# Kernel tuning notes

Measured on AMD Instinct MI355X. Metric: run time of the kernel, lower is better.

## Reference

```python
import jax, jax.numpy as jnp
import numpy as np

MAX_POS = 1024  # config.max_position_embeddings
NUM_HEADS = 16
HEAD_DIM = 64


def setup_inputs() -> dict:
    key = jax.random.key(0)
    ks = jax.random.split(key, 4)
    B, S, H = 4, 1024, 1024
    return {
        "hidden_states": jax.random.normal(ks[0], (B, S, H), dtype=jnp.float32),
        "qkv_w": jax.random.normal(ks[1], (3 * H, H), dtype=jnp.float32) * 0.02,
        "qkv_b": jax.random.normal(ks[2], (3 * H,), dtype=jnp.float32) * 0.02,
        "dist_emb": jax.random.normal(ks[3], (2 * MAX_POS - 1, HEAD_DIM), dtype=jnp.float32) * 0.02,
        "ext_mask": jnp.zeros((B, 1, 1, S), dtype=jnp.float32),
    }


def reference(hidden_states, qkv_w, qkv_b, dist_emb, ext_mask):
    B, S, H = hidden_states.shape
    h, d = NUM_HEADS, HEAD_DIM
    # fused QKV projection (q|k|v concatenated on output dim)
    qkv = jnp.einsum('bsi,oi->bso', hidden_states, qkv_w) + qkv_b
    q, k, v = jnp.split(qkv, 3, axis=-1)
    to_heads = lambda x: x.reshape(B, S, h, d).transpose(0, 2, 1, 3)  # [B,h,S,d]
    q, k, v = to_heads(q), to_heads(k), to_heads(v)
    # raw attention scores [B,h,S,S]
    scores = jnp.einsum('bhld,bhrd->bhlr', q, k)
    # relative_key_query positional bias
    pos = jnp.arange(S)
    distance = pos[:, None] - pos[None, :]          # [S,S]
    pe = dist_emb[distance + MAX_POS - 1]           # [S,S,d]
    scores = scores + jnp.einsum('bhld,lrd->bhlr', q, pe) \
                    + jnp.einsum('bhrd,lrd->bhlr', k, pe)
    scores = scores / jnp.sqrt(jnp.asarray(d, scores.dtype))
    scores = scores + ext_mask
    probs = jax.nn.softmax(scores, axis=-1)
    ctx = jnp.einsum('bhlr,bhrd->bhld', probs, v)   # [B,h,S,d]
    return ctx.transpose(0, 2, 1, 3).reshape(B, S, h * d)
```

## Files before the change

### kernel.cpp

```cpp
#include <hip/hip_runtime.h>
#include <hip/hip_bf16.h>

#define SEQ 1024
#define NH  16

typedef __attribute__((ext_vector_type(8))) short short8;
typedef __attribute__((ext_vector_type(4))) float floatx4;
typedef __attribute__((ext_vector_type(4))) unsigned short ushortx4;

#define GLDS16(gp, lp) __builtin_amdgcn_global_load_lds( \
    (const __attribute__((address_space(1))) void*)(gp), \
    (__attribute__((address_space(3))) void*)(lp), 16, 0, 0)

__device__ __forceinline__ unsigned short f2b(float f) {
    union { __hip_bfloat16 h; unsigned short u; } v;
    v.h = __float2bfloat16(f);
    return v.u;
}
__device__ __forceinline__ float b2f(unsigned short h) {
    union { unsigned u; float f; } v; v.u = ((unsigned)h) << 16;
    return v.f;
}

#define TADDR(base, row, ch) ((base) + ((row) << 6) + ((((ch) ^ ((row) & 7))) << 3))

__global__ void cast_kernel(const float* __restrict__ hs, const float* __restrict__ W,
                            const float* __restrict__ E,
                            unsigned short* __restrict__ hsb,
                            unsigned short* __restrict__ Wb,
                            unsigned short* __restrict__ Eb)
{
    const int QH = 1048576, QW = 786432, QE = 32752;
    const int NT = QH + QW + QE;
    for (int q = blockIdx.x * 256 + threadIdx.x; q < NT; q += gridDim.x * 256) {
        const float* src; unsigned short* dst; int off;
        if (q < QH)           { src = hs; dst = hsb; off = q; }
        else if (q < QH + QW) { src = W;  dst = Wb;  off = q - QH; }
        else                  { src = E;  dst = Eb;  off = q - QH - QW; }
        const float4 v = *(const float4*)(src + (size_t)off * 4);
        ushortx4 o; o[0] = f2b(v.x); o[1] = f2b(v.y); o[2] = f2b(v.z); o[3] = f2b(v.w);
        *(ushortx4*)(dst + (size_t)off * 4) = o;
    }
}

__global__ __launch_bounds__(256, 3) void qkv_gemm(
    const unsigned short* __restrict__ Ab, const unsigned short* __restrict__ Bb,
    const float* __restrict__ bias,
    unsigned short* __restrict__ Qb, unsigned short* __restrict__ Kb,
    unsigned short* __restrict__ Vt)
{
    __shared__ unsigned short sm[16384];
    const int t = threadIdx.x, w = t >> 6;
    const int ln = t & 15, g = (t >> 4) & 3;
    const int wm = w >> 1, wn = w & 1;
    const int bid = blockIdx.x + blockIdx.y * 24;
    const int swzid = (bid & 7) * 96 + (bid >> 3);
    const int m0 = (swzid / 24) << 7, o0 = (swzid % 24) << 7;

    floatx4 acc[4][4];
#pragma unroll
    for (int i = 0; i < 4; ++i)
#pragma unroll
        for (int j = 0; j < 4; ++j) acc[i][j] = (floatx4){0.f, 0.f, 0.f, 0.f};

    auto stage = [&](int kb, int buf) {
        const int base = buf << 14;
#pragma unroll
        for (int p = 0; p < 2; ++p) {
            const int idx = (p << 8) + t;
            const int row = idx >> 2;
            const int c = (idx & 3) ^ ((row ^ (row >> 2)) & 3);
            GLDS16(Ab + (size_t)(m0 + row) * 1024 + kb + (c << 3),
                   (char*)sm + base + (p << 12) + (w << 10));
            GLDS16(Bb + (size_t)(o0 + row) * 1024 + kb + (c << 3),
                   (char*)sm + base + 8192 + (p << 12) + (w << 10));
        }
    };

    stage(0, 0);
    __syncthreads();
    int buf = 0;
    for (int kb = 0; kb < 1024; kb += 32) {
        if (kb + 32 < 1024) stage(kb + 32, buf ^ 1);
        const int be = buf << 13;
        short8 af[4], bf_[4];
#pragma unroll
        for (int i = 0; i < 4; ++i) {
            const int r = (wm << 6) + (i << 4) + ln;
            af[i] = *(const short8*)&sm[be + (r << 5) + ((g ^ ((r ^ (r >> 2)) & 3)) << 3)];
        }
#pragma unroll
        for (int j = 0; j < 4; ++j) {
            const int r = (wn << 6) + (j << 4) + ln;
            bf_[j] = *(const short8*)&sm[be + 4096 + (r << 5) + ((g ^ ((r ^ (r >> 2)) & 3)) << 3)];
        }
#pragma unroll
        for (int i = 0; i < 4; ++i)
#pragma unroll
            for (int j = 0; j < 4; ++j)
                acc[i][j] = __builtin_amdgcn_mfma_f32_16x16x32_bf16(af[i], bf_[j], acc[i][j], 0, 0, 0);
        __syncthreads();
        buf ^= 1;
    }

    const int which = o0 >> 10;
    float bj[4];
#pragma unroll
    for (int j = 0; j < 4; ++j) bj[j] = bias[o0 + (wn << 6) + (j << 4) + ln];
    const int b0 = m0 >> 10;

    if (which == 2) {
#pragma unroll
        for (int i = 0; i < 4; ++i)
#pragma unroll
            for (int j = 0; j < 4; ++j) {
                const int oi = (wn << 6) + (j << 4) + ln;
                const int sb = oi & 15;
#pragma unroll
                for (int q = 0; q < 4; ++q) {
                    const int mi = (wm << 6) + (i << 4) + (g << 2) + q;
                    sm[(oi << 7) + ((((mi >> 3) ^ sb)) << 3) + (mi & 7)] =
                        f2b(acc[i][j][q] + bj[j]);
                }
            }
        __syncthreads();
#pragma unroll
        for (int it = 0; it < 8; ++it) {
            const int c = (it << 8) + t;
            const int oi = c >> 4, mi0 = (c & 15) << 3;
            const short8 v = *(const short8*)&sm[(oi << 7) + ((((mi0 >> 3) ^ (oi & 15))) << 3)];
            const int hh = ((o0 >> 6) + (oi >> 6)) & 15;
            const int d = oi & 63;
            const int s0 = (m0 & 1023) + mi0;
            *(short8*)(Vt + (((size_t)((b0 << 4) + hh)) << 16) + (d << 10) + s0) = v;
        }
    } else {
        unsigned short* dst = which ? Kb : Qb;
        const float sc = which ? 1.0f : 0.125f;
#pragma unroll
        for (int i = 0; i < 4; ++i)
#pragma unroll
            for (int j = 0; j < 4; ++j) {
                const int oi = (wn << 6) + (j << 4) + ln;
#pragma unroll
                for (int q = 0; q < 4; ++q) {
                    const int mi = (wm << 6) + (i << 4) + (g << 2) + q;
                    sm[(mi << 7) + oi] = f2b((acc[i][j][q] + bj[j]) * sc);
                }
            }
        __syncthreads();
#pragma unroll
        for (int it = 0; it < 8; ++it) {
            const int c = (it << 8) + t;
            const int mi = c >> 4, oi0 = (c & 15) << 3;
            const short8 v = *(const short8*)&sm[(mi << 7) + oi0];
            const int s = (m0 & 1023) + mi;
            const int hh = ((o0 >> 6) + (oi0 >> 6)) & 15;
            const int d0 = oi0 & 63;
            *(short8*)(dst + (((size_t)((b0 << 4) + hh)) << 16) + (s << 6) + d0) = v;
        }
    }
}

__global__ __launch_bounds__(256, 3) void attn_mfma(
    const unsigned short* __restrict__ Qb, const unsigned short* __restrict__ Kb,
    const unsigned short* __restrict__ Vt, const unsigned short* __restrict__ Eb,
    const float* __restrict__ mask, float* __restrict__ outp)
{
    __shared__ __align__(16) unsigned short sm[25600];
    const int t = threadIdx.x, w = t >> 6;
    const int wu = __builtin_amdgcn_readfirstlane(w);
    const int ln = t & 15, g = (t >> 4) & 3;
    const int bid = blockIdx.x;
    const int swz = ((bid & 7) << 7) | (bid >> 3);
    const int bh = swz >> 4;
    const int l0 = (swz & 15) << 6;
    const int b = bh >> 4, h = bh & 15;
    const size_t hb = (size_t)bh << 16;
    const int x0 = (w << 4) + (g << 2);

    const int qr = (w << 4) + ln;
    const short8 qa0 = *(const short8*)(Qb + hb + ((size_t)(l0 + qr) << 6) + (g << 3));
    const short8 qa1 = *(const short8*)(Qb + hb + ((size_t)(l0 + qr) << 6) + 32 + (g << 3));

    floatx4 O[4];
    float mr[4], lr[4];
#pragma unroll
    for (int dt = 0; dt < 4; ++dt) O[dt] = (floatx4){0.f, 0.f, 0.f, 0.f};
#pragma unroll
    for (int q = 0; q < 4; ++q) { mr[q] = -1e30f; lr[q] = 0.f; }

    for (int r0 = 0; r0 < SEQ; r0 += 64) {
        __syncthreads();
#pragma unroll
        for (int p = 0; p < 2; ++p) {
            const int idx = (p << 8) + t;
            const int row = idx >> 3;
            const int c = (idx & 7) ^ (row & 7);
            GLDS16(Kb + hb + ((size_t)(r0 + row) << 6) + (c << 3),
                   (char*)sm + (p << 12) + (w << 10));
        }
        const int j0 = l0 - r0 + 960;
#pragma unroll
        for (int p = 0; p < 4; ++p) {
            const int idx = (p << 8) + t;
            const int row = idx >> 3;
            const int c = (idx & 7) ^ (row & 7);
            GLDS16(Eb + ((size_t)(j0 + row) << 6) + (c << 3),
                   (char*)sm + 8192 + (p << 12) + (w << 10));
        }
        __syncthreads();
        short8 kf[4][2];
#pragma unroll
        for (int j = 0; j < 4; ++j) {
            const int kr = (j << 4) + ln;
            kf[j][0] = *(const short8*)&sm[TADDR(0, kr, g)];
            kf[j][1] = *(const short8*)&sm[TADDR(0, kr, 4 + g)];
        }
        const int wr = (w << 4) + ln;
        const short8 ka0 = *(const short8*)&sm[TADDR(0, wr, g)];
        const short8 ka1 = *(const short8*)&sm[TADDR(0, wr, 4 + g)];

        floatx4 S[4];
#pragma unroll
        for (int j = 0; j < 4; ++j) {
            floatx4 z = (floatx4){0.f, 0.f, 0.f, 0.f};
            z = __builtin_amdgcn_mfma_f32_16x16x32_bf16(qa0, kf[j][0], z, 0, 0, 0);
            S[j] = __builtin_amdgcn_mfma_f32_16x16x32_bf16(qa1, kf[j][1], z, 0, 0, 0);
        }
#pragma unroll
        for (int dt = 0; dt < 8; ++dt) {
            const bool doU = (dt >= wu) && (dt <= wu + 4);
            const bool doW = (dt >= 3 - wu) && (dt <= 7 - wu);
            if (!doU && !doW) continue;
            const int er = (dt << 4) + ln;
            const short8 e0 = *(const short8*)&sm[TADDR(4096, er, g)];
            const short8 e1 = *(const short8*)&sm[TADDR(4096, er, 4 + g)];
            if (doU) {
                floatx4 z = (floatx4){0.f, 0.f, 0.f, 0.f};
                z = __builtin_amdgcn_mfma_f32_16x16x32_bf16(qa0, e0, z, 0, 0, 0);
                const floatx4 U = __builtin_amdgcn_mfma_f32_16x16x32_bf16(qa1, e1, z, 0, 0, 0);
                int a = 12288 + (x0 - (dt << 4) - ln + 79) * 72 + x0;
#pragma unroll
                for (int q = 0; q < 4; ++q) { sm[a] = f2b(U[q]); a += 73; }
            }
            if (doW) {
                floatx4 z2 = (floatx4){0.f, 0.f, 0.f, 0.f};
                z2 = __builtin_amdgcn_mfma_f32_16x16x32_bf16(ka0, e0, z2, 0, 0, 0);
                const floatx4 Wv = __builtin_amdgcn_mfma_f32_16x16x32_bf16(ka1, e1, z2, 0, 0, 0);
                int a = 19200 + x0 * 101 + (dt << 4) + ln - 47;
#pragma unroll
                for (int q = 0; q < 4; ++q) { sm[a] = f2b(Wv[q] * 0.125f); a += 101; }
            }
        }
        __syncthreads();
#pragma unroll
        for (int p = 0; p < 2; ++p) {
            const int idx = (p << 8) + t;
            const int row = idx >> 3;
            const int c = (idx & 7) ^ (row & 7);
            GLDS16(Vt + hb + ((size_t)row << 10) + r0 + (c << 3),
                   (char*)sm + 8192 + (p << 12) + (w << 10));
        }
        float Pw[4][4];
#pragma unroll
        for (int j = 0; j < 4; ++j) {
            const int rr = (j << 4) + ln;
            const float mk = mask[(b << 10) + r0 + rr];
            const ushortx4 u4 = *(const ushortx4*)&sm[12288 + (rr + 16) * 72 + x0];
            const ushortx4 w4 = *(const ushortx4*)&sm[19200 + rr * 100 + 16 + x0];
#pragma unroll
            for (int q = 0; q < 4; ++q)
                S[j][q] += b2f(u4[q]) + b2f(w4[q]) + mk;
        }
#pragma unroll
        for (int q = 0; q < 4; ++q) {
            float tm = fmaxf(fmaxf(S[0][q], S[1][q]), fmaxf(S[2][q], S[3][q]));
            tm = fmaxf(tm, __shfl_xor(tm, 1));
            tm = fmaxf(tm, __shfl_xor(tm, 2));
            tm = fmaxf(tm, __shfl_xor(tm, 4));
            tm = fmaxf(tm, __shfl_xor(tm, 8));
            const float mnew = fmaxf(mr[q], tm);
            const float al = __expf(mr[q] - mnew);
            float sum = 0.f;
#pragma unroll
            for (int j = 0; j < 4; ++j) {
                const float p = __expf(S[j][q] - mnew);
                Pw[j][q] = p; sum += p;
            }
            sum += __shfl_xor(sum, 1);
            sum += __shfl_xor(sum, 2);
            sum += __shfl_xor(sum, 4);
            sum += __shfl_xor(sum, 8);
            lr[q] = lr[q] * al + sum;
            mr[q] = mnew;
#pragma unroll
            for (int dt = 0; dt < 4; ++dt) O[dt][q] *= al;
        }
#pragma unroll
        for (int j = 0; j < 4; ++j) {
            const int rr = (j << 4) + ln;
#pragma unroll
            for (int q = 0; q < 4; ++q) {
                const int l = x0 + q;
                sm[8192 + (l << 6) + ((((rr >> 3) ^ (l & 7)) << 3)) + (rr & 7)] = f2b(Pw[j][q]);
            }
        }
        __syncthreads();
        const int pr = (w << 4) + ln;
        const short8 pa0 = *(const short8*)&sm[TADDR(8192, pr, g)];
        const short8 pa1 = *(const short8*)&sm[TADDR(8192, pr, 4 + g)];
#pragma unroll
        for (int dt = 0; dt < 4; ++dt) {
            const int vr = (dt << 4) + ln;
            const short8 v0 = *(const short8*)&sm[TADDR(4096, vr, g)];
            const short8 v1 = *(const short8*)&sm[TADDR(4096, vr, 4 + g)];
            O[dt] = __builtin_amdgcn_mfma_f32_16x16x32_bf16(pa0, v0, O[dt], 0, 0, 0);
            O[dt] = __builtin_amdgcn_mfma_f32_16x16x32_bf16(pa1, v1, O[dt], 0, 0, 0);
        }
    }
#pragma unroll
    for (int dt = 0; dt < 4; ++dt)
#pragma unroll
        for (int q = 0; q < 4; ++q) {
            const int l = x0 + q;
            outp[((size_t)b << 20) + ((size_t)(l0 + l) << 10) + (h << 6) + (dt << 4) + ln]
                = O[dt][q] / lr[q];
        }
}

extern "C" void kernel_launch(void* const* d_in, const int* in_sizes, int n_in,
                              void* d_out, int out_size, void* d_ws, size_t ws_size,
                              hipStream_t stream)
{
    const float* hs   = (const float*)d_in[0];
    const float* qkvw = (const float*)d_in[1];
    const float* qkvb = (const float*)d_in[2];
    const float* demb = (const float*)d_in[3];
    const float* mask = (const float*)d_in[4];
    float* out = (float*)d_out;

    char* ws = (char*)d_ws;
    unsigned short* hsb = (unsigned short*)(ws);
    unsigned short* Wb  = (unsigned short*)(ws + 8388608);
    unsigned short* Eb  = (unsigned short*)(ws + 14680064);
    unsigned short* Qb  = (unsigned short*)(ws + 14942208);
    unsigned short* Kb  = (unsigned short*)(ws + 23330816);
    unsigned short* Vt  = (unsigned short*)(ws + 31719424);

    cast_kernel<<<2048, 256, 0, stream>>>(hs, qkvw, demb, hsb, Wb, Eb);
    qkv_gemm<<<dim3(24, 32), 256, 0, stream>>>(hsb, Wb, qkvb, Qb, Kb, Vt);
    attn_mfma<<<1024, 256, 0, stream>>>(Qb, Kb, Vt, Eb, mask, out);
}
```

Baseline: 226.8 us.

## Double-buffer K tiles and compact swizzled layout for relative-position bias staging

K tiles are now double-buffered in shared memory, and the next tile is prefetched during the softmax and PV phase so its load overlaps compute. The U/W positional-bias scratch buffers are repacked into compact 64x64 XOR-swizzled layouts that drop out-of-range entries. This frees LDS for the second K buffer and is meant to reduce bank conflicts on the bias writes and reads. It adds bounds checks on the bias stores and a more involved shared-memory address map.

Result: slower. 324.2 us (+43.0%).

```diff
diff --git a/kernel.cpp b/kernel.cpp
--- a/kernel.cpp
+++ b/kernel.cpp
@@ -167,7 +167,7 @@
     const unsigned short* __restrict__ Vt, const unsigned short* __restrict__ Eb,
     const float* __restrict__ mask, float* __restrict__ outp)
 {
-    __shared__ __align__(16) unsigned short sm[25600];
+    __shared__ __align__(16) unsigned short sm[24576];
     const int t = threadIdx.x, w = t >> 6;
     const int wu = __builtin_amdgcn_readfirstlane(w);
     const int ln = t & 15, g = (t >> 4) & 3;
@@ -178,28 +178,35 @@
     const int b = bh >> 4, h = bh & 15;
     const size_t hb = (size_t)bh << 16;
     const int x0 = (w << 4) + (g << 2);
+    const int cb = x0 >> 2;
 
     const int qr = (w << 4) + ln;
     const short8 qa0 = *(const short8*)(Qb + hb + ((size_t)(l0 + qr) << 6) + (g << 3));
     const short8 qa1 = *(const short8*)(Qb + hb + ((size_t)(l0 + qr) << 6) + 32 + (g << 3));
 
-    floatx4 O[4];
-    float mr[4], lr[4];
-#pragma unroll
-    for (int dt = 0; dt < 4; ++dt) O[dt] = (floatx4){0.f, 0.f, 0.f, 0.f};
-#pragma unroll
-    for (int q = 0; q < 4; ++q) { mr[q] = -1e30f; lr[q] = 0.f; }
-
-    for (int r0 = 0; r0 < SEQ; r0 += 64) {
-        __syncthreads();
+    auto stageK = [&](int rb, int kbuf) {
 #pragma unroll
         for (int p = 0; p < 2; ++p) {
             const int idx = (p << 8) + t;
             const int row = idx >> 3;
             const int c = (idx & 7) ^ (row & 7);
-            GLDS16(Kb + hb + ((size_t)(r0 + row) << 6) + (c << 3),
-                   (char*)sm + (p << 12) + (w << 10));
-        }
+            GLDS16(Kb + hb + ((size_t)(rb + row) << 6) + (c << 3),
+                   (char*)sm + (kbuf << 13) + (p << 12) + (w << 10));
+        }
+    };
+
+    stageK(0, 0);
+
+    floatx4 O[4];
+    float mr[4], lr[4];
+#pragma unroll
+    for (int dt = 0; dt < 4; ++dt) O[dt] = (floatx4){0.f, 0.f, 0.f, 0.f};
+#pragma unroll
+    for (int q = 0; q < 4; ++q) { mr[q] = -1e30f; lr[q] = 0.f; }
+
+    for (int r0 = 0; r0 < SEQ; r0 += 64) {
+        const int kb = (r0 >> 6) & 1;
+        __syncthreads();
         const int j0 = l0 - r0 + 960;
 #pragma unroll
         for (int p = 0; p < 4; ++p) {
@@ -207,19 +214,20 @@
             const int row = idx >> 3;
             const int c = (idx & 7) ^ (row & 7);
             GLDS16(Eb + ((size_t)(j0 + row) << 6) + (c << 3),
-                   (char*)sm + 8192 + (p << 12) + (w << 10));
-        }
-        __syncthreads();
+                   (char*)sm + 16384 + (p << 12) + (w << 10));
+        }
+        __syncthreads();
+        const int kbase = kb << 12;
         short8 kf[4][2];
 #pragma unroll
         for (int j = 0; j < 4; ++j) {
             const int kr = (j << 4) + ln;
-            kf[j][0] = *(const short8*)&sm[TADDR(0, kr, g)];
-            kf[j][1] = *(const short8*)&sm[TADDR(0, kr, 4 + g)];
+            kf[j][0] = *(const short8*)&sm[TADDR(kbase, kr, g)];
+            kf[j][1] = *(const short8*)&sm[TADDR(kbase, kr, 4 + g)];
         }
         const int wr = (w << 4) + ln;
-        const short8 ka0 = *(const short8*)&sm[TADDR(0, wr, g)];
-        const short8 ka1 = *(const short8*)&sm[TADDR(0, wr, 4 + g)];
+        const short8 ka0 = *(const short8*)&sm[TADDR(kbase, wr, g)];
+        const short8 ka1 = *(const short8*)&sm[TADDR(kbase, wr, 4 + g)];
 
         floatx4 S[4];
 #pragma unroll
@@ -234,41 +242,53 @@
             const bool doW = (dt >= 3 - wu) && (dt <= 7 - wu);
             if (!doU && !doW) continue;
             const int er = (dt << 4) + ln;
-            const short8 e0 = *(const short8*)&sm[TADDR(4096, er, g)];
-            const short8 e1 = *(const short8*)&sm[TADDR(4096, er, 4 + g)];
+            const short8 e0 = *(const short8*)&sm[TADDR(8192, er, g)];
+            const short8 e1 = *(const short8*)&sm[TADDR(8192, er, 4 + g)];
             if (doU) {
                 floatx4 z = (floatx4){0.f, 0.f, 0.f, 0.f};
                 z = __builtin_amdgcn_mfma_f32_16x16x32_bf16(qa0, e0, z, 0, 0, 0);
                 const floatx4 U = __builtin_amdgcn_mfma_f32_16x16x32_bf16(qa1, e1, z, 0, 0, 0);
-                int a = 12288 + (x0 - (dt << 4) - ln + 79) * 72 + x0;
-#pragma unroll
-                for (int q = 0; q < 4; ++q) { sm[a] = f2b(U[q]); a += 73; }
+#pragma unroll
+                for (int q = 0; q < 4; ++q) {
+                    const int ru = x0 + q - (dt << 4) - ln + 63;
+                    if ((unsigned)ru < 64u)
+                        sm[16384 + (ru << 6) + ((cb ^ (ru & 15)) << 2) + q] = f2b(U[q]);
+                }
             }
             if (doW) {
                 floatx4 z2 = (floatx4){0.f, 0.f, 0.f, 0.f};
                 z2 = __builtin_amdgcn_mfma_f32_16x16x32_bf16(ka0, e0, z2, 0, 0, 0);
                 const floatx4 Wv = __builtin_amdgcn_mfma_f32_16x16x32_bf16(ka1, e1, z2, 0, 0, 0);
-                int a = 19200 + x0 * 101 + (dt << 4) + ln - 47;
-#pragma unroll
-                for (int q = 0; q < 4; ++q) { sm[a] = f2b(Wv[q] * 0.125f); a += 101; }
-            }
-        }
-        __syncthreads();
+#pragma unroll
+                for (int q = 0; q < 4; ++q) {
+                    const int r = x0 + q;
+                    const int lw = (dt << 4) + ln + r - 63;
+                    if ((unsigned)lw < 64u)
+                        sm[20480 + (r << 6) + (((lw >> 2) ^ (r & 15)) << 2) + (lw & 3)]
+                            = f2b(Wv[q] * 0.125f);
+                }
+            }
+        }
+        __syncthreads();
+
 #pragma unroll
         for (int p = 0; p < 2; ++p) {
             const int idx = (p << 8) + t;
             const int row = idx >> 3;
             const int c = (idx & 7) ^ (row & 7);
             GLDS16(Vt + hb + ((size_t)row << 10) + r0 + (c << 3),
-                   (char*)sm + 8192 + (p << 12) + (w << 10));
-        }
+                   (char*)sm + 16384 + (p << 12) + (w << 10));
+        }
+        if (r0 < 960) stageK(r0 + 64, kb ^ 1);
+
         float Pw[4][4];
 #pragma unroll
         for (int j = 0; j < 4; ++j) {
             const int rr = (j << 4) + ln;
             const float mk = mask[(b << 10) + r0 + rr];
-            const ushortx4 u4 = *(const ushortx4*)&sm[12288 + (rr + 16) * 72 + x0];
-            const ushortx4 w4 = *(const ushortx4*)&sm[19200 + rr * 100 + 16 + x0];
+            const int sa = (rr << 6) + ((cb ^ (rr & 15)) << 2);
+            const ushortx4 u4 = *(const ushortx4*)&sm[16384 + sa];
+            const ushortx4 w4 = *(const ushortx4*)&sm[20480 + sa];
 #pragma unroll
             for (int q = 0; q < 4; ++q)
                 S[j][q] += b2f(u4[q]) + b2f(w4[q]) + mk;
@@ -303,18 +323,19 @@
 #pragma unroll
             for (int q = 0; q < 4; ++q) {
                 const int l = x0 + q;
-                sm[8192 + (l << 6) + ((((rr >> 3) ^ (l & 7)) << 3)) + (rr & 7)] = f2b(Pw[j][q]);
-            }
-        }
-        __syncthreads();
+                sm[12288 + (l << 6) + ((((rr >> 3) ^ (l & 7)) << 3)) + (rr & 7)] = f2b(Pw[j][q]);
+            }
+        }
+        __syncthreads();
+
         const int pr = (w << 4) + ln;
-        const short8 pa0 = *(const short8*)&sm[TADDR(8192, pr, g)];
-        const short8 pa1 = *(const short8*)&sm[TADDR(8192, pr, 4 + g)];
+        const short8 pa0 = *(const short8*)&sm[TADDR(12288, pr, g)];
+        const short8 pa1 = *(const short8*)&sm[TADDR(12288, pr, 4 + g)];
 #pragma unroll
         for (int dt = 0; dt < 4; ++dt) {
             const int vr = (dt << 4) + ln;
-            const short8 v0 = *(const short8*)&sm[TADDR(4096, vr, g)];
-            const short8 v1 = *(const short8*)&sm[TADDR(4096, vr, 4 + g)];
+            const short8 v0 = *(const short8*)&sm[TADDR(8192, vr, g)];
+            const short8 v1 = *(const short8*)&sm[TADDR(8192, vr, 4 + g)];
             O[dt] = __builtin_amdgcn_mfma_f32_16x16x32_bf16(pa0, v0, O[dt], 0, 0, 0);
             O[dt] = __builtin_amdgcn_mfma_f32_16x16x32_bf16(pa1, v1, O[dt], 0, 0, 0);
         }
```

## Split attention key range in two blocks and merge partial softmax results

Applied to the files above, without the earlier changes.

The attention kernel now launches twice as many blocks, each covering half of the key sequence, and writes unnormalized partial outputs plus row max and sum. A new merge kernel combines the two halves with log-sum-exp rescaling. The aim is more blocks to fill the GPU's compute units (1024 blocks at 3 per CU), in exchange for an extra kernel launch and extra global traffic for the partial outputs. The first partial buffer aliases the final output, and the merge reads and writes it in place element-wise.

Result: no change. 222.9 us (-1.7%).

```diff
diff --git a/kernel.cpp b/kernel.cpp
--- a/kernel.cpp
+++ b/kernel.cpp
@@ -162,22 +162,28 @@
     }
 }
 
-__global__ __launch_bounds__(256, 3) void attn_mfma(
+__global__ __launch_bounds__(256, 3) void attn_split(
     const unsigned short* __restrict__ Qb, const unsigned short* __restrict__ Kb,
     const unsigned short* __restrict__ Vt, const unsigned short* __restrict__ Eb,
-    const float* __restrict__ mask, float* __restrict__ outp)
+    const float* __restrict__ mask,
+    float* __restrict__ pO0, float* __restrict__ pO1,
+    float* __restrict__ mA, float* __restrict__ lA,
+    float* __restrict__ mB, float* __restrict__ lB)
 {
     __shared__ __align__(16) unsigned short sm[25600];
     const int t = threadIdx.x, w = t >> 6;
     const int wu = __builtin_amdgcn_readfirstlane(w);
     const int ln = t & 15, g = (t >> 4) & 3;
     const int bid = blockIdx.x;
-    const int swz = ((bid & 7) << 7) | (bid >> 3);
-    const int bh = swz >> 4;
-    const int l0 = (swz & 15) << 6;
+    const int u = ((bid & 7) << 8) + (bid >> 3);
+    const int half = u & 1;
+    const int rest = u >> 1;
+    const int bh = rest >> 4;
+    const int l0 = (rest & 15) << 6;
     const int b = bh >> 4, h = bh & 15;
     const size_t hb = (size_t)bh << 16;
     const int x0 = (w << 4) + (g << 2);
+    const int r0beg = half << 9, r0end = (half << 9) + 512;
 
     const int qr = (w << 4) + ln;
     const short8 qa0 = *(const short8*)(Qb + hb + ((size_t)(l0 + qr) << 6) + (g << 3));
@@ -190,7 +196,7 @@
 #pragma unroll
     for (int q = 0; q < 4; ++q) { mr[q] = -1e30f; lr[q] = 0.f; }
 
-    for (int r0 = 0; r0 < SEQ; r0 += 64) {
+    for (int r0 = r0beg; r0 < r0end; r0 += 64) {
         __syncthreads();
 #pragma unroll
         for (int p = 0; p < 2; ++p) {
@@ -319,14 +325,45 @@
             O[dt] = __builtin_amdgcn_mfma_f32_16x16x32_bf16(pa1, v1, O[dt], 0, 0, 0);
         }
     }
+    float* pDst = half ? pO1 : pO0;
+    float* mDst = half ? mB : mA;
+    float* lDst = half ? lB : lA;
 #pragma unroll
     for (int dt = 0; dt < 4; ++dt)
 #pragma unroll
         for (int q = 0; q < 4; ++q) {
             const int l = x0 + q;
-            outp[((size_t)b << 20) + ((size_t)(l0 + l) << 10) + (h << 6) + (dt << 4) + ln]
-                = O[dt][q] / lr[q];
-        }
+            pDst[((size_t)b << 20) + ((size_t)(l0 + l) << 10) + (h << 6) + (dt << 4) + ln]
+                = O[dt][q];
+        }
+    if (ln == 0) {
+        const int rowbase = (bh << 10) + l0 + x0;
+#pragma unroll
+        for (int q = 0; q < 4; ++q) { mDst[rowbase + q] = mr[q]; lDst[rowbase + q] = lr[q]; }
+    }
+}
+
+__global__ void merge_kernel(const float* __restrict__ pO0, const float* __restrict__ pO1,
+                             const float* __restrict__ mA, const float* __restrict__ lA,
+                             const float* __restrict__ mB, const float* __restrict__ lB,
+                             float* __restrict__ outp)
+{
+    const int idx = blockIdx.x * 256 + threadIdx.x;
+    const int rowg = idx >> 4, d4 = (idx & 15) << 2;
+    const int b = rowg >> 14, h = (rowg >> 10) & 15, l = rowg & 1023;
+    const size_t off = ((size_t)b << 20) + ((size_t)l << 10) + (h << 6) + d4;
+    const float m1 = mA[rowg], m2 = mB[rowg];
+    const float mm = fmaxf(m1, m2);
+    const float a1 = __expf(m1 - mm), a2 = __expf(m2 - mm);
+    const float inv = 1.f / (a1 * lA[rowg] + a2 * lB[rowg]);
+    const float4 o1 = *(const float4*)(pO0 + off);
+    const float4 o2 = *(const float4*)(pO1 + off);
+    float4 r;
+    r.x = (a1 * o1.x + a2 * o2.x) * inv;
+    r.y = (a1 * o1.y + a2 * o2.y) * inv;
+    r.z = (a1 * o1.z + a2 * o2.z) * inv;
+    r.w = (a1 * o1.w + a2 * o2.w) * inv;
+    *(float4*)(outp + off) = r;
 }
 
 extern "C" void kernel_launch(void* const* d_in, const int* in_sizes, int n_in,
@@ -347,8 +384,14 @@
     unsigned short* Qb  = (unsigned short*)(ws + 14942208);
     unsigned short* Kb  = (unsigned short*)(ws + 23330816);
     unsigned short* Vt  = (unsigned short*)(ws + 31719424);
+    float* pO1 = (float*)(ws + 40108032);
+    float* mA  = (float*)(ws + 56885248);
+    float* lA  = (float*)(ws + 57147392);
+    float* mB  = (float*)(ws + 57409536);
+    float* lB  = (float*)(ws + 57671680);
 
     cast_kernel<<<2048, 256, 0, stream>>>(hs, qkvw, demb, hsb, Wb, Eb);
     qkv_gemm<<<dim3(24, 32), 256, 0, stream>>>(hsb, Wb, qkvb, Qb, Kb, Vt);
-    attn_mfma<<<1024, 256, 0, stream>>>(Qb, Kb, Vt, Eb, mask, out);
-}
+    attn_split<<<2048, 256, 0, stream>>>(Qb, Kb, Vt, Eb, mask, out, pO1, mA, lA, mB, lB);
+    merge_kernel<<<4096, 256, 0, stream>>>(out, pO1, mA, lA, mB, lB, out);
+}
```

## Split attention key range across blocks and merge partial softmax results

Applied to the files above, without the earlier changes.

Splits each attention query tile's key loop into 2 or 3 pieces run by separate blocks, writing unnormalized partial outputs plus row max and sum to workspace. A new merge kernel rescales and combines the partials into the final output. The aim is more blocks and better occupancy and load balance across the CUs, since 1024 blocks may underfill the GPU. The cost is extra global traffic for the partials and one more kernel launch.

Result: slower. 236.3 us (+4.2%).

```diff
diff --git a/kernel.cpp b/kernel.cpp
--- a/kernel.cpp
+++ b/kernel.cpp
@@ -162,22 +162,29 @@
     }
 }
 
-__global__ __launch_bounds__(256, 3) void attn_mfma(
+__global__ __launch_bounds__(256, 3) void attn_split(
     const unsigned short* __restrict__ Qb, const unsigned short* __restrict__ Kb,
     const unsigned short* __restrict__ Vt, const unsigned short* __restrict__ Eb,
-    const float* __restrict__ mask, float* __restrict__ outp)
+    const float* __restrict__ mask,
+    float* __restrict__ pO0, float* __restrict__ pOx,
+    float* __restrict__ mArr, float* __restrict__ lArr, int np)
 {
     __shared__ __align__(16) unsigned short sm[25600];
     const int t = threadIdx.x, w = t >> 6;
     const int wu = __builtin_amdgcn_readfirstlane(w);
     const int ln = t & 15, g = (t >> 4) & 3;
     const int bid = blockIdx.x;
-    const int swz = ((bid & 7) << 7) | (bid >> 3);
-    const int bh = swz >> 4;
-    const int l0 = (swz & 15) << 6;
+    const int chunk = gridDim.x >> 3;
+    const int u = (bid & 7) * chunk + (bid >> 3);
+    const int piece = u >> 10;
+    const int rest = u & 1023;
+    const int bh = rest >> 4;
+    const int l0 = (rest & 15) << 6;
     const int b = bh >> 4, h = bh & 15;
     const size_t hb = (size_t)bh << 16;
     const int x0 = (w << 4) + (g << 2);
+    const int r0beg = ((piece * 16) / np) << 6;
+    const int r0end = (((piece + 1) * 16) / np) << 6;
 
     const int qr = (w << 4) + ln;
     const short8 qa0 = *(const short8*)(Qb + hb + ((size_t)(l0 + qr) << 6) + (g << 3));
@@ -190,7 +197,7 @@
 #pragma unroll
     for (int q = 0; q < 4; ++q) { mr[q] = -1e30f; lr[q] = 0.f; }
 
-    for (int r0 = 0; r0 < SEQ; r0 += 64) {
+    for (int r0 = r0beg; r0 < r0end; r0 += 64) {
         __syncthreads();
 #pragma unroll
         for (int p = 0; p < 2; ++p) {
@@ -319,14 +326,46 @@
             O[dt] = __builtin_amdgcn_mfma_f32_16x16x32_bf16(pa1, v1, O[dt], 0, 0, 0);
         }
     }
+    float* pDst = piece ? (pOx + (size_t)(piece - 1) * 4194304) : pO0;
+    float* mDst = mArr + (size_t)piece * 65536;
+    float* lDst = lArr + (size_t)piece * 65536;
 #pragma unroll
     for (int dt = 0; dt < 4; ++dt)
 #pragma unroll
         for (int q = 0; q < 4; ++q) {
             const int l = x0 + q;
-            outp[((size_t)b << 20) + ((size_t)(l0 + l) << 10) + (h << 6) + (dt << 4) + ln]
-                = O[dt][q] / lr[q];
-        }
+            pDst[((size_t)b << 20) + ((size_t)(l0 + l) << 10) + (h << 6) + (dt << 4) + ln]
+                = O[dt][q];
+        }
+    if (ln == 0) {
+        const int rowbase = (bh << 10) + l0 + x0;
+#pragma unroll
+        for (int q = 0; q < 4; ++q) { mDst[rowbase + q] = mr[q]; lDst[rowbase + q] = lr[q]; }
+    }
+}
+
+__global__ void merge_kernel(const float* __restrict__ pO0, const float* __restrict__ pOx,
+                             const float* __restrict__ mArr, const float* __restrict__ lArr,
+                             float* __restrict__ outp, int np)
+{
+    const int idx = blockIdx.x * 256 + threadIdx.x;
+    const int rowg = idx >> 4, d4 = (idx & 15) << 2;
+    const int b = rowg >> 14, h = (rowg >> 10) & 15, l = rowg & 1023;
+    const size_t off = ((size_t)b << 20) + ((size_t)l << 10) + (h << 6) + d4;
+    float mm = -1e30f;
+    for (int p = 0; p < np; ++p) mm = fmaxf(mm, mArr[p * 65536 + rowg]);
+    float denom = 0.f;
+    float4 acc = {0.f, 0.f, 0.f, 0.f};
+    for (int p = 0; p < np; ++p) {
+        const float a = __expf(mArr[p * 65536 + rowg] - mm);
+        denom += a * lArr[p * 65536 + rowg];
+        const float* src = p ? (pOx + (size_t)(p - 1) * 4194304) : pO0;
+        const float4 o = *(const float4*)(src + off);
+        acc.x += a * o.x; acc.y += a * o.y; acc.z += a * o.z; acc.w += a * o.w;
+    }
+    const float inv = 1.f / denom;
+    float4 r; r.x = acc.x * inv; r.y = acc.y * inv; r.z = acc.z * inv; r.w = acc.w * inv;
+    *(float4*)(outp + off) = r;
 }
 
 extern "C" void kernel_launch(void* const* d_in, const int* in_sizes, int n_in,
@@ -347,8 +386,14 @@
     unsigned short* Qb  = (unsigned short*)(ws + 14942208);
     unsigned short* Kb  = (unsigned short*)(ws + 23330816);
     unsigned short* Vt  = (unsigned short*)(ws + 31719424);
+    float* pOx = (float*)(ws + 40108032);
+
+    const int np = (ws_size >= 75235328) ? 3 : 2;
+    float* mArr = (np == 3) ? (float*)(ws + 73662464) : (float*)(ws + 56885248);
+    float* lArr = (np == 3) ? (float*)(ws + 74448896) : (float*)(ws + 57409536);
 
     cast_kernel<<<2048, 256, 0, stream>>>(hs, qkvw, demb, hsb, Wb, Eb);
     qkv_gemm<<<dim3(24, 32), 256, 0, stream>>>(hsb, Wb, qkvb, Qb, Kb, Vt);
-    attn_mfma<<<1024, 256, 0, stream>>>(Qb, Kb, Vt, Eb, mask, out);
-}
+    attn_split<<<1024 * np, 256, 0, stream>>>(Qb, Kb, Vt, Eb, mask, out, pOx, mArr, lArr, np);
+    merge_kernel<<<4096, 256, 0, stream>>>(out, pOx, mArr, lArr, out, np);
+}
```
